# Kernel optimization log

Hardware: AMD Instinct MI355X
Metric: run time of the kernel (lower is better)

Reference implementation:

```python
import jax, jax.numpy as jnp
from jax import lax
import numpy as np

B = 4096          # batch
EMBED = 32        # embed_dim
HEADS = 2
MEM_SIZE = 4096
MEM_DIM = 256
TOPK = 10
LN_EPS = 1e-5


def setup_inputs() -> dict:
    key = jax.random.key(0)
    ks = jax.random.split(key, 32)
    rn = lambda i, shape, s=0.05: (jax.random.normal(ks[i], shape) * s).astype(jnp.float32)
    return {
        'x': jax.random.normal(ks[0], (B, 1, 28, 28), dtype=jnp.float32),
        'patch_w': rn(1, (32, 1, 4, 4)), 'patch_b': rn(2, (32,)),
        'blk_ln1_g': jnp.ones((2, 32), jnp.float32), 'blk_ln1_b': jnp.zeros((2, 32), jnp.float32),
        'blk_inproj_w': rn(3, (2, 96, 32)), 'blk_inproj_b': rn(4, (2, 96)),
        'blk_outproj_w': rn(5, (2, 32, 32)), 'blk_outproj_b': rn(6, (2, 32)),
        'blk_ln2_g': jnp.ones((2, 32), jnp.float32), 'blk_ln2_b': jnp.zeros((2, 32), jnp.float32),
        'blk_ff1_w': rn(7, (2, 128, 32)), 'blk_ff1_b': rn(8, (2, 128)),
        'blk_ff2_w': rn(9, (2, 32, 128)), 'blk_ff2_b': rn(10, (2, 32)),
        'lat_w': rn(11, (256, 1568)), 'lat_b': rn(12, (256,)),
        'memory': jax.random.normal(ks[13], (MEM_SIZE, MEM_DIM), dtype=jnp.float32),
        'dec_w': rn(14, (3136, 256)), 'dec_b': rn(15, (3136,)),
        'upt1_w': rn(16, (64, 32, 4, 4)), 'upt1_b': rn(17, (32,)),
        'c1_w': rn(18, (32, 32, 3, 3)), 'c1_b': rn(19, (32,)),
        'upt2_w': rn(20, (32, 16, 4, 4)), 'upt2_b': rn(21, (16,)),
        'c2_w': rn(22, (8, 16, 3, 3)), 'c2_b': rn(23, (8,)),
        'c3_w': rn(24, (1, 8, 1, 1)), 'c3_b': rn(25, (1,)),
    }


def _ln(x, g, b):
    m = jnp.mean(x, -1, keepdims=True)
    v = jnp.mean((x - m) ** 2, -1, keepdims=True)
    return (x - m) / jnp.sqrt(v + LN_EPS) * g + b


def _conv2d(x, w, b, stride=1, pad=0):
    out = lax.conv_general_dilated(x, w, (stride, stride), ((pad, pad), (pad, pad)),
                                   dimension_numbers=('NCHW', 'OIHW', 'NCHW'))
    return out + b[None, :, None, None]


def _conv_transpose2d(x, w, b, stride, pad):
    # w in torch layout [in, out, kh, kw]; equivalent fractionally-strided conv
    w_f = jnp.flip(w, (2, 3)).transpose(1, 0, 2, 3)  # OIHW
    k = w.shape[2]
    p = k - 1 - pad
    out = lax.conv_general_dilated(x, w_f, (1, 1), ((p, p), (p, p)),
                                   lhs_dilation=(stride, stride),
                                   dimension_numbers=('NCHW', 'OIHW', 'NCHW'))
    return out + b[None, :, None, None]


def _mha(x, wi, bi, wo, bo):
    Bn, S, D = x.shape
    Dh = D // HEADS
    qkv = x @ wi.T + bi                                  # [B,S,3D]
    q, k, v = jnp.split(qkv, 3, axis=-1)
    sp = lambda t: t.reshape(Bn, S, HEADS, Dh).transpose(0, 2, 1, 3)
    q, k, v = sp(q), sp(k), sp(v)
    scores = jnp.einsum('bhqd,bhkd->bhqk', q, k) / jnp.sqrt(jnp.asarray(Dh, x.dtype))
    att = jax.nn.softmax(scores, axis=-1)
    o = jnp.einsum('bhqk,bhkd->bhqd', att, v).transpose(0, 2, 1, 3).reshape(Bn, S, D)
    return o @ wo.T + bo


def _memory_read(latent, memory):
    # cosine-sim topk softmax-weighted gather (F.normalize eps=1e-12)
    mn = memory / jnp.clip(jnp.linalg.norm(memory, axis=1, keepdims=True), 1e-12)
    xn = latent / jnp.clip(jnp.linalg.norm(latent, axis=1, keepdims=True), 1e-12)
    sim = xn @ mn.T                                       # [B, MEM_SIZE]
    topk_sim, topk_idx = lax.top_k(sim, TOPK)
    w = jax.nn.softmax(topk_sim, axis=1)                  # [B, TOPK]
    sel = memory[topk_idx]                                # [B, TOPK, MEM_DIM]
    return jnp.einsum('bk,bkd->bd', w, sel)


def _forward(x, patch_w, patch_b, blk_ln1_g, blk_ln1_b, blk_inproj_w, blk_inproj_b,
             blk_outproj_w, blk_outproj_b, blk_ln2_g, blk_ln2_b, blk_ff1_w, blk_ff1_b,
             blk_ff2_w, blk_ff2_b, lat_w, lat_b, memory, dec_w, dec_b,
             upt1_w, upt1_b, c1_w, c1_b, upt2_w, upt2_b, c2_w, c2_b, c3_w, c3_b):
    Bn = x.shape[0]
    h = _conv2d(x, patch_w, patch_b, stride=4)            # [B,32,7,7]
    t = h.reshape(Bn, EMBED, 49).transpose(0, 2, 1)       # [B,49,32]
    for i in range(2):                                    # two SwinBlocks
        t = t + _mha(_ln(t, blk_ln1_g[i], blk_ln1_b[i]),
                     blk_inproj_w[i], blk_inproj_b[i], blk_outproj_w[i], blk_outproj_b[i])
        f = _ln(t, blk_ln2_g[i], blk_ln2_b[i])
        f = jax.nn.gelu(f @ blk_ff1_w[i].T + blk_ff1_b[i], approximate=False)
        t = t + (f @ blk_ff2_w[i].T + blk_ff2_b[i])
    latent = t.reshape(Bn, -1) @ lat_w.T + lat_b          # [B,256]
    mem_latent = _memory_read(latent, memory)             # [B,256]
    d = (mem_latent @ dec_w.T + dec_b).reshape(Bn, 64, 7, 7)  # dropout=eval identity
    d = jax.nn.relu(_conv_transpose2d(d, upt1_w, upt1_b, 2, 1))   # [B,32,14,14]
    d = jax.nn.relu(_conv2d(d, c1_w, c1_b, 1, 1))
    d = jax.nn.relu(_conv_transpose2d(d, upt2_w, upt2_b, 2, 1))   # [B,16,28,28]
    d = jax.nn.relu(_conv2d(d, c2_w, c2_b, 1, 1))                 # [B,8,28,28]
    return _conv2d(d, c3_w, c3_b, 1, 0)                           # [B,1,28,28]


def reference(x, patch_w, patch_b, blk_ln1_g, blk_ln1_b, blk_inproj_w, blk_inproj_b,
              blk_outproj_w, blk_outproj_b, blk_ln2_g, blk_ln2_b, blk_ff1_w, blk_ff1_b,
              blk_ff2_w, blk_ff2_b, lat_w, lat_b, memory, dec_w, dec_b,
              upt1_w, upt1_b, c1_w, c1_b, upt2_w, upt2_b, c2_w, c2_b, c3_w, c3_b):
    return _forward(x, patch_w, patch_b, blk_ln1_g, blk_ln1_b, blk_inproj_w, blk_inproj_b,
                    blk_outproj_w, blk_outproj_b, blk_ln2_g, blk_ln2_b, blk_ff1_w, blk_ff1_b,
                    blk_ff2_w, blk_ff2_b, lat_w, lat_b, memory, dec_w, dec_b,
                    upt1_w, upt1_b, c1_w, c1_b, upt2_w, upt2_b, c2_w, c2_b, c3_w, c3_b)
```

## Files before the change

### kernel.cpp

```cpp
#include <hip/hip_runtime.h>
#include <math.h>

#define B_TOT 4096
#define CHUNK 4096

typedef _Float16 half_t;
typedef _Float16 h2 __attribute__((ext_vector_type(2)));
typedef _Float16 h8v __attribute__((ext_vector_type(8)));
typedef float f4v __attribute__((ext_vector_type(4)));
typedef float f2v __attribute__((ext_vector_type(2)));

#if __has_builtin(__builtin_amdgcn_fdot2)
#define FDOT2(a, b, c) __builtin_amdgcn_fdot2((a), (b), (c), false)
#else
#define FDOT2(a, b, c) fmaf((float)(a)[1], (float)(b)[1], fmaf((float)(a)[0], (float)(b)[0], (c)))
#endif

#define KSTR 36
#define VSTR 34
#define KBYTES (49 * 72)
#define WAVE_LDS (49 * 72 + 49 * 136)
#define WI_OFF  (4 * WAVE_LDS)
#define BLOCK_LDS (WI_OFF + 12288)

__global__ __launch_bounds__(256) void k_tokens(
    const float* __restrict__ x, const float* __restrict__ pw, const float* __restrict__ pb,
    const float* __restrict__ ln1g, const float* __restrict__ ln1b,
    const float* __restrict__ wi, const float* __restrict__ bi,
    const float* __restrict__ wo, const float* __restrict__ bo,
    const float* __restrict__ ln2g, const float* __restrict__ ln2b,
    const float* __restrict__ w1, const float* __restrict__ fb1,
    const float* __restrict__ w2t, const float* __restrict__ fb2,
    float* __restrict__ tokens)
{
    __shared__ __align__(16) unsigned char Lraw[BLOCK_LDS];
    const int tid = threadIdx.x;
    const int wv = tid >> 6, lane = tid & 63;
    const int b = blockIdx.x * 4 + wv;
    half_t* Kb = (half_t*)(Lraw + wv * WAVE_LDS);
    float*  Vb = (float*)(Lraw + wv * WAVE_LDS + KBYTES);
    const float* wiL = (const float*)(Lraw + WI_OFF);
    float* Lf = (float*)Lraw;
    const bool is_tok = lane < 49;
    const int s = is_tok ? lane : 48;
    const int py = s / 7, px = s % 7;

    {
        const float4* srcw = (const float4*)(wi);
        float4* dstw = (float4*)(Lraw + WI_OFF);
        for (int e = tid; e < 768; e += 256) dstw[e] = srcw[e];
    }

    f2v xv2[8];
    const float* xb = x + (size_t)b * 784 + py * 112 + px * 4;
    #pragma unroll
    for (int r = 0; r < 4; ++r) {
        float4 vq = *(const float4*)(xb + r * 28);
        f2v lo; lo[0] = vq.x; lo[1] = vq.y;
        f2v hi; hi[0] = vq.z; hi[1] = vq.w;
        xv2[2 * r] = lo; xv2[2 * r + 1] = hi;
    }
    f2v t2[16];
    #pragma unroll
    for (int c = 0; c < 32; ++c) {
        const float* wr = pw + c * 16;
        f2v a2 = (f2v){0.f, 0.f};
        #pragma unroll
        for (int c2 = 0; c2 < 4; ++c2) {
            float4 wq = *(const float4*)&wr[4 * c2];
            f2v w0; w0[0] = wq.x; w0[1] = wq.y;
            f2v w1v; w1v[0] = wq.z; w1v[1] = wq.w;
            a2 += xv2[2 * c2] * w0;
            a2 += xv2[2 * c2 + 1] * w1v;
        }
        t2[c >> 1][c & 1] = pb[c] + a2[0] + a2[1];
    }

    for (int blk = 0; blk < 2; ++blk) {
        const float* bib = bi + blk * 96;

        f2v mu2 = (f2v){0.f, 0.f};
        #pragma unroll
        for (int i = 0; i < 16; ++i) mu2 += t2[i];
        float mu = (mu2[0] + mu2[1]) * 0.03125f;
        f2v mub; mub[0] = mu; mub[1] = mu;
        f2v var2 = (f2v){0.f, 0.f};
        #pragma unroll
        for (int i = 0; i < 16; ++i) { f2v d = t2[i] - mub; var2 += d * d; }
        float rstd = rsqrtf((var2[0] + var2[1]) * 0.03125f + 1e-5f);
        f2v rstd2; rstd2[0] = rstd; rstd2[1] = rstd;
        f2v xn2[16];
        {
            const f2v* g2 = (const f2v*)(ln1g + blk * 32);
            const f2v* bl2 = (const f2v*)(ln1b + blk * 32);
            #pragma unroll
            for (int i = 0; i < 16; ++i)
                xn2[i] = (t2[i] - mub) * rstd2 * g2[i] + bl2[i];
        }

        __syncthreads();

        #pragma unroll 4
        for (int d = 0; d < 32; ++d) {
            const float* wr = wiL + (32 + d) * 32;
            f2v a2 = (f2v){0.f, 0.f};
            #pragma unroll
            for (int c2 = 0; c2 < 8; ++c2) {
                float4 wq = *(const float4*)&wr[4 * c2];
                f2v w0; w0[0] = wq.x; w0[1] = wq.y;
                f2v w1v; w1v[0] = wq.z; w1v[1] = wq.w;
                a2 += xn2[2 * c2] * w0;
                a2 += xn2[2 * c2 + 1] * w1v;
            }
            if (is_tok) Kb[s * KSTR + d] = (half_t)(bib[32 + d] + a2[0] + a2[1]);
        }
        #pragma unroll 4
        for (int d = 0; d < 32; ++d) {
            const float* wr = wiL + (64 + d) * 32;
            f2v a2 = (f2v){0.f, 0.f};
            #pragma unroll
            for (int c2 = 0; c2 < 8; ++c2) {
                float4 wq = *(const float4*)&wr[4 * c2];
                f2v w0; w0[0] = wq.x; w0[1] = wq.y;
                f2v w1v; w1v[0] = wq.z; w1v[1] = wq.w;
                a2 += xn2[2 * c2] * w0;
                a2 += xn2[2 * c2 + 1] * w1v;
            }
            if (is_tok) Vb[s * VSTR + d] = bib[64 + d] + a2[0] + a2[1];
        }
        float q0[32];
        #pragma unroll 4
        for (int d = 0; d < 32; ++d) {
            const float* wr = wiL + d * 32;
            f2v a2 = (f2v){0.f, 0.f};
            #pragma unroll
            for (int c2 = 0; c2 < 8; ++c2) {
                float4 wq = *(const float4*)&wr[4 * c2];
                f2v w0; w0[0] = wq.x; w0[1] = wq.y;
                f2v w1v; w1v[0] = wq.z; w1v[1] = wq.w;
                a2 += xn2[2 * c2] * w0;
                a2 += xn2[2 * c2 + 1] * w1v;
            }
            q0[d] = (bib[d] + a2[0] + a2[1]) * 0.25f;
        }
        h2 qh[16];
        #pragma unroll
        for (int i = 0; i < 16; ++i) {
            h2 hh; hh[0] = (half_t)q0[2 * i]; hh[1] = (half_t)q0[2 * i + 1];
            qh[i] = hh;
        }

        __asm__ volatile("s_waitcnt lgkmcnt(0)" ::: "memory");

        f2v o2[16];
        #pragma unroll
        for (int i = 0; i < 16; ++i) o2[i] = (f2v){0.f, 0.f};
        float l0 = 0.f, l1 = 0.f;
        union H4 { double qd; h2 p[2]; };
        for (int j = 0; j < 49; ++j) {
            const double* kr = (const double*)(Kb + j * KSTR);
            const float* vr = Vb + j * VSTR;
            H4 u0, u1, u2, u3, w0, w1h, w2h, w3;
            u0.qd = kr[0]; u1.qd = kr[1]; u2.qd = kr[2]; u3.qd = kr[3];
            w0.qd = kr[4]; w1h.qd = kr[5]; w2h.qd = kr[6]; w3.qd = kr[7];
            float s0a = 0.f, s0b = 0.f, s1a = 0.f, s1b = 0.f;
            s0a = FDOT2(u0.p[0], qh[0], s0a); s0a = FDOT2(u0.p[1], qh[1], s0a);
            s0b = FDOT2(u1.p[0], qh[2], s0b); s0b = FDOT2(u1.p[1], qh[3], s0b);
            s0a = FDOT2(u2.p[0], qh[4], s0a); s0a = FDOT2(u2.p[1], qh[5], s0a);
            s0b = FDOT2(u3.p[0], qh[6], s0b); s0b = FDOT2(u3.p[1], qh[7], s0b);
            s1a = FDOT2(w0.p[0], qh[8], s1a); s1a = FDOT2(w0.p[1], qh[9], s1a);
            s1b = FDOT2(w1h.p[0], qh[10], s1b); s1b = FDOT2(w1h.p[1], qh[11], s1b);
            s1a = FDOT2(w2h.p[0], qh[12], s1a); s1a = FDOT2(w2h.p[1], qh[13], s1a);
            s1b = FDOT2(w3.p[0], qh[14], s1b); s1b = FDOT2(w3.p[1], qh[15], s1b);
            float p0 = __expf(s0a + s0b), p1 = __expf(s1a + s1b);
            l0 += p0; l1 += p1;
            f2v p02; p02[0] = p0; p02[1] = p0;
            f2v p12; p12[0] = p1; p12[1] = p1;
            #pragma unroll
            for (int i = 0; i < 8; ++i) {
                f2v va = *(const f2v*)&vr[2 * i];
                o2[i] += p02 * va;
                f2v vc = *(const f2v*)&vr[16 + 2 * i];
                o2[8 + i] += p12 * vc;
            }
        }
        {
            float il0 = 1.f / l0, il1 = 1.f / l1;
            f2v il02; il02[0] = il0; il02[1] = il0;
            f2v il12; il12[0] = il1; il12[1] = il1;
            #pragma unroll
            for (int i = 0; i < 8; ++i) { o2[i] *= il02; o2[8 + i] *= il12; }
        }

        #pragma unroll
        for (int c = 0; c < 32; ++c) {
            const float* wr = wo + blk * 1024 + c * 32;
            f2v a2 = (f2v){0.f, 0.f};
            #pragma unroll
            for (int c2 = 0; c2 < 8; ++c2) {
                float4 wq = *(const float4*)&wr[4 * c2];
                f2v w0; w0[0] = wq.x; w0[1] = wq.y;
                f2v w1v; w1v[0] = wq.z; w1v[1] = wq.w;
                a2 += o2[2 * c2] * w0;
                a2 += o2[2 * c2 + 1] * w1v;
            }
            t2[c >> 1][c & 1] += bo[blk * 32 + c] + a2[0] + a2[1];
        }

        mu2 = (f2v){0.f, 0.f};
        #pragma unroll
        for (int i = 0; i < 16; ++i) mu2 += t2[i];
        mu = (mu2[0] + mu2[1]) * 0.03125f;
        mub[0] = mu; mub[1] = mu;
        var2 = (f2v){0.f, 0.f};
        #pragma unroll
        for (int i = 0; i < 16; ++i) { f2v d = t2[i] - mub; var2 += d * d; }
        rstd = rsqrtf((var2[0] + var2[1]) * 0.03125f + 1e-5f);
        rstd2[0] = rstd; rstd2[1] = rstd;
        {
            const f2v* g2 = (const f2v*)(ln2g + blk * 32);
            const f2v* bl2 = (const f2v*)(ln2b + blk * 32);
            #pragma unroll
            for (int i = 0; i < 16; ++i)
                xn2[i] = (t2[i] - mub) * rstd2 * g2[i] + bl2[i];
        }

        __syncthreads();

        {
            const float4* src1 = (const float4*)(w1 + blk * 4096);
            const float4* src2 = (const float4*)(w2t + blk * 4096);
            float4* dst = (float4*)Lraw;
            for (int e = tid; e < 1024; e += 256) dst[e] = src1[e];
            for (int e = tid; e < 1024; e += 256) dst[1024 + e] = src2[e];
            if (blk == 0) {
                const float4* srcw = (const float4*)(wi + 3072);
                float4* dstw = (float4*)(Lraw + WI_OFF);
                for (int e = tid; e < 768; e += 256) dstw[e] = srcw[e];
            }
        }
        __syncthreads();

        const float* w2L = Lf + 4096;
        #pragma unroll 2
        for (int j = 0; j < 128; ++j) {
            const float* wr = Lf + j * 32;
            f2v h2a = (f2v){0.f, 0.f};
            #pragma unroll
            for (int c2 = 0; c2 < 8; ++c2) {
                float4 wq = *(const float4*)&wr[4 * c2];
                f2v w0; w0[0] = wq.x; w0[1] = wq.y;
                f2v w1v; w1v[0] = wq.z; w1v[1] = wq.w;
                h2a += xn2[2 * c2] * w0;
                h2a += xn2[2 * c2 + 1] * w1v;
            }
            float h = fb1[blk * 128 + j] + h2a[0] + h2a[1];
            h = 0.5f * h * (1.f + erff(h * 0.7071067811865476f));
            f2v hh; hh[0] = h; hh[1] = h;
            const float* w2r = w2L + j * 32;
            #pragma unroll
            for (int c2 = 0; c2 < 8; ++c2) {
                float4 wq = *(const float4*)&w2r[4 * c2];
                f2v w0; w0[0] = wq.x; w0[1] = wq.y;
                f2v w1v; w1v[0] = wq.z; w1v[1] = wq.w;
                t2[2 * c2]     += hh * w0;
                t2[2 * c2 + 1] += hh * w1v;
            }
        }
        {
            const f2v* fb22 = (const f2v*)(fb2 + blk * 32);
            #pragma unroll
            for (int i = 0; i < 16; ++i) t2[i] += fb22[i];
        }
    }

    if (is_tok) {
        float* op = tokens + (size_t)b * 1568 + s * 32;
        #pragma unroll
        for (int i = 0; i < 8; ++i) {
            float4 vv = make_float4(t2[2 * i][0], t2[2 * i][1],
                                    t2[2 * i + 1][0], t2[2 * i + 1][1]);
            *(float4*)&op[4 * i] = vv;
        }
    }
}

__global__ __launch_bounds__(256) void k_split(
    const float* __restrict__ lat_w, const float* __restrict__ memory,
    half_t* __restrict__ lwh, half_t* __restrict__ lwl,
    half_t* __restrict__ memh, half_t* __restrict__ meml)
{
    size_t i = (size_t)blockIdx.x * 256 + threadIdx.x;
    if (i < 401408) {
        float v = lat_w[i];
        half_t h = (half_t)v;
        lwh[i] = h; lwl[i] = (half_t)((v - (float)h) * 2048.0f);
    }
    if (i < 1048576) {
        float v = memory[i];
        half_t h = (half_t)v;
        memh[i] = h; meml[i] = (half_t)((v - (float)h) * 2048.0f);
    }
}

__global__ __launch_bounds__(256) void k_sgemm(
    const float* __restrict__ A, const half_t* __restrict__ Bhg,
    const half_t* __restrict__ Blg, const float* __restrict__ bias,
    float* __restrict__ C, int M, int N, int K)
{
    __shared__ __align__(16) half_t Ah[64 * 40];
    __shared__ __align__(16) half_t Al[64 * 40];
    __shared__ __align__(16) half_t Bh[128 * 40];
    __shared__ __align__(16) half_t Bl[128 * 40];
    const int tid = threadIdx.x;
    const int n0 = blockIdx.x * 128, m0 = blockIdx.y * 64;
    const int w = tid >> 6, lane = tid & 63;
    const int wm = (w >> 1) * 32, wn = (w & 1) * 64;
    const int lr = lane & 15, lk = lane >> 4;

    const int ar = tid >> 2, aseg = (tid & 3) * 8;
    const int br = tid >> 1, bseg = (tid & 1) * 16;

    f4v acch[2][4], accm[2][4];
    #pragma unroll
    for (int i = 0; i < 2; ++i)
        #pragma unroll
        for (int j = 0; j < 4; ++j) {
            acch[i][j] = (f4v){0.f, 0.f, 0.f, 0.f};
            accm[i][j] = (f4v){0.f, 0.f, 0.f, 0.f};
        }

    for (int k0 = 0; k0 < K; k0 += 32) {
        {
            const float* ap = A + (size_t)(m0 + ar) * K + k0 + aseg;
            float4 a0 = *(const float4*)ap;
            float4 a1 = *(const float4*)(ap + 4);
            float av[8] = {a0.x, a0.y, a0.z, a0.w, a1.x, a1.y, a1.z, a1.w};
            h8v ah, al;
            #pragma unroll
            for (int i = 0; i < 8; ++i) {
                half_t h = (half_t)av[i];
                ah[i] = h;
                al[i] = (half_t)((av[i] - (float)h) * 2048.0f);
            }
            *(h8v*)&Ah[ar * 40 + aseg] = ah;
            *(h8v*)&Al[ar * 40 + aseg] = al;

            const half_t* bph = Bhg + (size_t)(n0 + br) * K + k0 + bseg;
            const half_t* bpl = Blg + (size_t)(n0 + br) * K + k0 + bseg;
            h8v bh0 = *(const h8v*)bph;
            h8v bh1 = *(const h8v*)(bph + 8);
            h8v bl0 = *(const h8v*)bpl;
            h8v bl1 = *(const h8v*)(bpl + 8);
            *(h8v*)&Bh[br * 40 + bseg]     = bh0;
            *(h8v*)&Bh[br * 40 + bseg + 8] = bh1;
            *(h8v*)&Bl[br * 40 + bseg]     = bl0;
            *(h8v*)&Bl[br * 40 + bseg + 8] = bl1;
        }
        __syncthreads();
        h8v afh[2], afl[2], bfh[4], bfl[4];
        #pragma unroll
        for (int i = 0; i < 2; ++i) {
            afh[i] = *(const h8v*)&Ah[(wm + i * 16 + lr) * 40 + lk * 8];
            afl[i] = *(const h8v*)&Al[(wm + i * 16 + lr) * 40 + lk * 8];
        }
        #pragma unroll
        for (int j = 0; j < 4; ++j) {
            bfh[j] = *(const h8v*)&Bh[(wn + j * 16 + lr) * 40 + lk * 8];
            bfl[j] = *(const h8v*)&Bl[(wn + j * 16 + lr) * 40 + lk * 8];
        }
        #pragma unroll
        for (int i = 0; i < 2; ++i)
            #pragma unroll
            for (int j = 0; j < 4; ++j) {
                acch[i][j] = __builtin_amdgcn_mfma_f32_16x16x32_f16(afh[i], bfh[j], acch[i][j], 0, 0, 0);
                accm[i][j] = __builtin_amdgcn_mfma_f32_16x16x32_f16(afh[i], bfl[j], accm[i][j], 0, 0, 0);
                accm[i][j] = __builtin_amdgcn_mfma_f32_16x16x32_f16(afl[i], bfh[j], accm[i][j], 0, 0, 0);
            }
        __syncthreads();
    }

    #pragma unroll
    for (int j = 0; j < 4; ++j) {
        int n = n0 + wn + j * 16 + lr;
        float bv = bias ? bias[n] : 0.f;
        #pragma unroll
        for (int i = 0; i < 2; ++i) {
            #pragma unroll
            for (int r = 0; r < 4; ++r) {
                int m = m0 + wm + i * 16 + lk * 4 + r;
                C[(size_t)m * N + n] = acch[i][j][r] + accm[i][j][r] * (1.0f / 2048.0f) + bv;
            }
        }
    }
}

__global__ __launch_bounds__(256) void k_dgemm(
    const float* __restrict__ A, const float* __restrict__ Bm,
    const float* __restrict__ bias, half_t* __restrict__ C,
    int M, int N, int K)
{
    __shared__ __align__(16) half_t As[64 * 40];
    __shared__ __align__(16) half_t Bs[128 * 40];
    const int tid = threadIdx.x;
    const int n0 = blockIdx.x * 128, m0 = blockIdx.y * 64;
    const int w = tid >> 6, lane = tid & 63;
    const int wm = (w >> 1) * 32, wn = (w & 1) * 64;
    const int lr = lane & 15, lk = lane >> 4;

    const int ar = tid >> 2, aseg = (tid & 3) * 8;
    const int br = tid >> 1, bseg = (tid & 1) * 16;

    f4v acc[2][4];
    #pragma unroll
    for (int i = 0; i < 2; ++i)
        #pragma unroll
        for (int j = 0; j < 4; ++j) acc[i][j] = (f4v){0.f, 0.f, 0.f, 0.f};

    for (int k0 = 0; k0 < K; k0 += 32) {
        {
            const float* ap = A + (size_t)(m0 + ar) * K + k0 + aseg;
            float4 a0 = *(const float4*)ap;
            float4 a1 = *(const float4*)(ap + 4);
            h8v ha;
            ha[0] = (half_t)a0.x; ha[1] = (half_t)a0.y;
            ha[2] = (half_t)a0.z; ha[3] = (half_t)a0.w;
            ha[4] = (half_t)a1.x; ha[5] = (half_t)a1.y;
            ha[6] = (half_t)a1.z; ha[7] = (half_t)a1.w;
            *(h8v*)&As[ar * 40 + aseg] = ha;

            const float* bp = Bm + (size_t)(n0 + br) * K + k0 + bseg;
            float4 b0 = *(const float4*)bp;
            float4 b1 = *(const float4*)(bp + 4);
            float4 b2 = *(const float4*)(bp + 8);
            float4 b3 = *(const float4*)(bp + 12);
            h8v hb0, hb1;
            hb0[0] = (half_t)b0.x; hb0[1] = (half_t)b0.y;
            hb0[2] = (half_t)b0.z; hb0[3] = (half_t)b0.w;
            hb0[4] = (half_t)b1.x; hb0[5] = (half_t)b1.y;
            hb0[6] = (half_t)b1.z; hb0[7] = (half_t)b1.w;
            hb1[0] = (half_t)b2.x; hb1[1] = (half_t)b2.y;
            hb1[2] = (half_t)b2.z; hb1[3] = (half_t)b2.w;
            hb1[4] = (half_t)b3.x; hb1[5] = (half_t)b3.y;
            hb1[6] = (half_t)b3.z; hb1[7] = (half_t)b3.w;
            *(h8v*)&Bs[br * 40 + bseg] = hb0;
            *(h8v*)&Bs[br * 40 + bseg + 8] = hb1;
        }
        __syncthreads();
        h8v af[2], bfr[4];
        #pragma unroll
        for (int i = 0; i < 2; ++i)
            af[i] = *(const h8v*)&As[(wm + i * 16 + lr) * 40 + lk * 8];
        #pragma unroll
        for (int j = 0; j < 4; ++j)
            bfr[j] = *(const h8v*)&Bs[(wn + j * 16 + lr) * 40 + lk * 8];
        #pragma unroll
        for (int i = 0; i < 2; ++i)
            #pragma unroll
            for (int j = 0; j < 4; ++j)
                acc[i][j] = __builtin_amdgcn_mfma_f32_16x16x32_f16(af[i], bfr[j], acc[i][j], 0, 0, 0);
        __syncthreads();
    }

    #pragma unroll
    for (int j = 0; j < 4; ++j) {
        int n = n0 + wn + j * 16 + lr;
        float bv = bias[n];
        #pragma unroll
        for (int i = 0; i < 2; ++i) {
            #pragma unroll
            for (int r = 0; r < 4; ++r) {
                int m = m0 + wm + i * 16 + lk * 4 + r;
                C[(size_t)m * N + n] = (half_t)fmaxf(acc[i][j][r] + bv, 0.f);
            }
        }
    }
}

__global__ __launch_bounds__(256) void k_fuse(
    const float* __restrict__ wt1, const float* __restrict__ upt1_b,
    const float* __restrict__ dec_w, const float* __restrict__ dec_b,
    float* __restrict__ Wf, float* __restrict__ bf)
{
    __shared__ float WL[4][64][32];
    const int p = blockIdx.x;
    const int k = threadIdx.x;
    const int y = p / 14, x = p % 14;

    int ky0 = 0, iy0 = 0, ky1 = 0, iy1 = 0, nky = 0;
    for (int ky = 0; ky < 4; ++ky) {
        int iyn = y + 1 - ky;
        if (iyn < 0 || (iyn & 1)) continue;
        int iy = iyn >> 1;
        if (iy > 6) continue;
        if (nky == 0) { ky0 = ky; iy0 = iy; } else { ky1 = ky; iy1 = iy; }
        ++nky;
    }
    int kx0 = 0, ix0 = 0, kx1 = 0, ix1 = 0, nkx = 0;
    for (int kx = 0; kx < 4; ++kx) {
        int ixn = x + 1 - kx;
        if (ixn < 0 || (ixn & 1)) continue;
        int ix = ixn >> 1;
        if (ix > 6) continue;
        if (nkx == 0) { kx0 = kx; ix0 = ix; } else { kx1 = kx; ix1 = ix; }
        ++nkx;
    }
    const int ntap = nky * nkx;

    for (int e = k; e < ntap * 2048; e += 256) {
        int t = e >> 11, c = (e >> 5) & 63, o = e & 31;
        int ti = (nkx == 2) ? (t >> 1) : t;
        int tj = (nkx == 2) ? (t & 1) : 0;
        int ky = ti ? ky1 : ky0;
        int kx = tj ? kx1 : kx0;
        WL[t][c][o] = wt1[((c * 32 + o) * 4 + ky) * 4 + kx];
    }
    __syncthreads();

    f2v acc2[16];
    #pragma unroll
    for (int o = 0; o < 16; ++o) acc2[o] = (f2v){0.f, 0.f};
    float bacc = 0.f;

    for (int t = 0; t < ntap; ++t) {
        int ti = (nkx == 2) ? (t >> 1) : t;
        int tj = (nkx == 2) ? (t & 1) : 0;
        int iy = ti ? iy1 : iy0;
        int ix = tj ? ix1 : ix0;
        int rbase = iy * 7 + ix;
        for (int c = 0; c < 64; ++c) {
            int row = c * 49 + rbase;
            float v = dec_w[(size_t)row * 256 + k];
            f2v vv; vv[0] = v; vv[1] = v;
            const f2v* w2p = (const f2v*)&WL[t][c][0];
            #pragma unroll
            for (int o2 = 0; o2 < 16; ++o2) acc2[o2] += vv * w2p[o2];
            if (k < 32) bacc = fmaf(WL[t][c][k], dec_b[row], bacc);
        }
    }

    #pragma unroll 4
    for (int o = 0; o < 32; ++o)
        Wf[((size_t)(p * 32 + o)) * 256 + k] = acc2[o >> 1][o & 1];
    if (k < 32) bf[p * 32 + k] = bacc + upt1_b[k];
}

__global__ __launch_bounds__(256) void k_mnorm(const float* __restrict__ mem, float* __restrict__ inv_norm)
{
    __shared__ float red[256];
    const int row = blockIdx.x, tid = threadIdx.x;
    float v = mem[(size_t)row * 256 + tid];
    red[tid] = v * v;
    __syncthreads();
    for (int s = 128; s > 0; s >>= 1) {
        if (tid < s) red[tid] += red[tid + s];
        __syncthreads();
    }
    if (tid == 0) inv_norm[row] = 1.f / fmaxf(sqrtf(red[0]), 1e-12f);
}

__global__ __launch_bounds__(256) void k_memread(
    const float* __restrict__ latent, const float* __restrict__ dots,
    const float* __restrict__ inv_mn, const float* __restrict__ mem,
    float* __restrict__ out)
{
    __shared__ float red[256];
    __shared__ int   redi[4];
    __shared__ float inv_x_s;
    const int b = blockIdx.x, tid = threadIdx.x;
    const int w = tid >> 6, lane = tid & 63;
    float lx = latent[(size_t)b * 256 + tid];
    red[tid] = lx * lx;
    __syncthreads();
    for (int s = 128; s > 0; s >>= 1) {
        if (tid < s) red[tid] += red[tid + s];
        __syncthreads();
    }
    if (tid == 0) inv_x_s = 1.f / fmaxf(sqrtf(red[0]), 1e-12f);
    __syncthreads();
    const float inv_x = inv_x_s;

    float vals[16];
    for (int j = 0; j < 16; ++j) {
        int m = tid + j * 256;
        vals[j] = dots[(size_t)b * 4096 + m] * inv_mn[m] * inv_x;
    }
    float tv[10]; int ti[10];
    for (int t = 0; t < 10; ++t) {
        float bv = -1e30f; int bidx = 0x7fffffff;
        #pragma unroll
        for (int j = 0; j < 16; ++j) {
            int m = tid + j * 256;
            float v = vals[j];
            if (v > bv || (v == bv && m < bidx)) { bv = v; bidx = m; }
        }
        #pragma unroll
        for (int off = 32; off > 0; off >>= 1) {
            float ov = __shfl_xor(bv, off);
            int   oi = __shfl_xor(bidx, off);
            if (ov > bv || (ov == bv && oi < bidx)) { bv = ov; bidx = oi; }
        }
        if (lane == 0) { red[w] = bv; redi[w] = bidx; }
        __syncthreads();
        float fv = red[0]; int fi = redi[0];
        #pragma unroll
        for (int q = 1; q < 4; ++q) {
            float v2 = red[q]; int i2 = redi[q];
            if (v2 > fv || (v2 == fv && i2 < fi)) { fv = v2; fi = i2; }
        }
        tv[t] = fv; ti[t] = fi;
        if ((fi & 255) == tid) vals[fi >> 8] = -1e30f;
        __syncthreads();
    }
    float wgt[10], wsum = 0.f;
    for (int t = 0; t < 10; ++t) { wgt[t] = expf(tv[t] - tv[0]); wsum += wgt[t]; }
    float inv_ws = 1.f / wsum;
    float acc = 0.f;
    for (int t = 0; t < 10; ++t) acc += (wgt[t] * inv_ws) * mem[(size_t)ti[t] * 256 + tid];
    out[(size_t)b * 256 + tid] = acc;
}

__global__ __launch_bounds__(256) void k_pack(
    const float* __restrict__ wc1, const float* __restrict__ wt2,
    const float* __restrict__ wc2, const float* __restrict__ w2src,
    half_t* __restrict__ pk2h, half_t* __restrict__ pk3h,
    float* __restrict__ pk4, float* __restrict__ pk5)
{
    int i = blockIdx.x * 256 + threadIdx.x;
    if (i < 9216) {
        int ic = i & 31, oc = (i >> 5) & 15, nt = (i >> 9) & 1, t = i >> 10;
        pk2h[i] = (half_t)wc1[((nt * 16 + oc) * 32 + ic) * 9 + t];
    }
    if (i < 8192) {
        int ic = i & 31, oc = (i >> 5) & 15, t = (i >> 9) & 3, q = i >> 11;
        int wy = t >> 1, wx = t & 1, py = q >> 1, px = q & 1;
        int ky = 3 - py - 2 * wy, kx = 3 - px - 2 * wx;
        pk3h[i] = (half_t)wt2[((ic * 16 + oc) * 4 + ky) * 4 + kx];
    }
    if (i < 1152) {
        int o = i & 7, tap = (i >> 3) % 9, c = i / 72;
        pk4[i] = wc2[(o * 16 + c) * 9 + tap];
    }
    if (i < 8192) {
        int c = i & 31, j = (i >> 5) & 127, bq = i >> 12;
        pk5[i] = w2src[bq * 4096 + c * 128 + j];
    }
}

__global__ __launch_bounds__(256) void k_conv1(
    const half_t* __restrict__ in, const half_t* __restrict__ wh,
    const float* __restrict__ bias, half_t* __restrict__ out)
{
    __shared__ __align__(16) half_t P[2 * 16 * 16 * 40];
    const int tid = threadIdx.x;
    const int w = tid >> 6, lane = tid & 63;
    const size_t b0 = (size_t)blockIdx.x * 2;

    for (int e = tid; e < 10240; e += 256) ((unsigned int*)P)[e] = 0u;
    __syncthreads();
    {
        const unsigned int* src = (const unsigned int*)in;
        for (int e = tid; e < 6272; e += 256) {
            int si = e / 3136;
            int rem = e - si * 3136;
            int p = rem >> 4, c2 = rem & 15;
            int y = p / 14, x = p % 14;
            ((unsigned int*)P)[si * 5120 + ((y + 1) * 16 + (x + 1)) * 20 + c2] =
                src[(b0 + si) * 3136 + rem];
        }
    }

    h8v bfr[9][2];
    #pragma unroll
    for (int t = 0; t < 9; ++t)
        #pragma unroll
        for (int nt = 0; nt < 2; ++nt)
            bfr[t][nt] = *(const h8v*)&wh[((size_t)((t * 2 + nt) * 16 + (lane & 15))) * 32 + (lane >> 4) * 8];

    __syncthreads();

    const int kseg = (lane >> 4) * 8;
    const int oc = lane & 15;
    const float bv0 = bias[oc], bv1 = bias[16 + oc];

    for (int job = w; job < 26; job += 4) {
        const int si = job >= 13 ? 1 : 0;
        const int tile = job - si * 13;
        int p = tile * 16 + (lane & 15);
        if (p > 195) p = 195;
        const int y = p / 14, x = p % 14;
        const half_t* Pb = P + si * 10240;

        f4v acc0 = (f4v){0.f, 0.f, 0.f, 0.f};
        f4v acc1 = (f4v){0.f, 0.f, 0.f, 0.f};
        #pragma unroll
        for (int ky = 0; ky < 3; ++ky) {
            #pragma unroll
            for (int kx = 0; kx < 3; ++kx) {
                h8v af = *(const h8v*)&Pb[((y + ky) * 16 + (x + kx)) * 40 + kseg];
                acc0 = __builtin_amdgcn_mfma_f32_16x16x32_f16(af, bfr[ky * 3 + kx][0], acc0, 0, 0, 0);
                acc1 = __builtin_amdgcn_mfma_f32_16x16x32_f16(af, bfr[ky * 3 + kx][1], acc1, 0, 0, 0);
            }
        }

        const int pr0 = tile * 16 + (lane >> 4) * 4;
        half_t* ob = out + (b0 + si) * 6272;
        #pragma unroll
        for (int r = 0; r < 4; ++r) {
            int pp = pr0 + r;
            if (pp < 196) {
                ob[(size_t)pp * 32 + oc]      = (half_t)fmaxf(acc0[r] + bv0, 0.f);
                ob[(size_t)pp * 32 + 16 + oc] = (half_t)fmaxf(acc1[r] + bv1, 0.f);
            }
        }
    }
}

__global__ __launch_bounds__(256) void k_convt23(
    const half_t* __restrict__ in, const half_t* __restrict__ pk3h,
    const float* __restrict__ bt2, const float* __restrict__ pk4,
    const float* __restrict__ b2, const float* __restrict__ w3,
    const float* __restrict__ b3, float* __restrict__ out)
{
    __shared__ __align__(16) unsigned char Lraw[30720];
    half_t* Pin = (half_t*)Lraw;
    float*  P2  = (float*)Lraw;
    const int tid = threadIdx.x;
    const int w = tid >> 6, lane = tid & 63;
    const int b = blockIdx.x;

    for (int e = tid; e < 5120; e += 256) ((unsigned int*)Pin)[e] = 0u;
    __syncthreads();
    {
        const unsigned int* src = (const unsigned int*)in;
        for (int e = tid; e < 3136; e += 256) {
            int p = e >> 4, c2 = e & 15;
            int y = p / 14, x = p % 14;
            ((unsigned int*)Pin)[((y + 1) * 16 + (x + 1)) * 20 + c2] =
                src[(size_t)b * 3136 + e];
        }
    }
    __syncthreads();

    const int oc = lane & 15;
    const int kseg = (lane >> 4) * 8;

    f4v res[13];
    #pragma unroll
    for (int j = 0; j < 13; ++j) {
        const int job = w + 4 * j;
        const int q = job / 13, tile = job - q * 13;
        const int py = q >> 1, px = q & 1;
        int p = tile * 16 + (lane & 15);
        if (p > 195) p = 195;
        const int ty = p / 14, tx = p % 14;
        f4v a = (f4v){0.f, 0.f, 0.f, 0.f};
        #pragma unroll
        for (int t = 0; t < 4; ++t) {
            const int wy = t >> 1, wx = t & 1;
            h8v bf = *(const h8v*)&pk3h[((size_t)((q * 4 + t) * 16 + oc)) * 32 + kseg];
            h8v af = *(const h8v*)&Pin[((ty + py + wy) * 16 + (tx + px + wx)) * 40 + kseg];
            a = __builtin_amdgcn_mfma_f32_16x16x32_f16(af, bf, a, 0, 0, 0);
        }
        res[j] = a;
    }
    __syncthreads();

    const bool active2 = tid < 196;
    int row = active2 ? tid / 7 : 0;
    int tx0b = active2 ? (tid % 7) * 4 : 0;
    const float bco = bt2[oc];

    f2v acc2[4][4];
    #pragma unroll
    for (int i = 0; i < 4; ++i)
        #pragma unroll
        for (int o2 = 0; o2 < 4; ++o2) acc2[i][o2] = (f2v){0.f, 0.f};

    #pragma unroll
    for (int g = 0; g < 2; ++g) {
        for (int e = tid; e < 7680; e += 256) P2[e] = 0.f;
        __syncthreads();
        if ((oc >> 3) == g) {
            #pragma unroll
            for (int j = 0; j < 13; ++j) {
                const int job = w + 4 * j;
                const int q = job / 13, tile = job - q * 13;
                const int py = q >> 1, px = q & 1;
                const int pr0 = tile * 16 + (lane >> 4) * 4;
                #pragma unroll
                for (int r = 0; r < 4; ++r) {
                    int p = pr0 + r;
                    if (p < 196) {
                        int Y = 2 * (p / 14) + py, X = 2 * (p % 14) + px;
                        P2[((oc & 7) * 30 + Y + 1) * 32 + (X + 1)] = fmaxf(res[j][r] + bco, 0.f);
                    }
                }
            }
        }
        __syncthreads();
        for (int cl = 0; cl < 8; ++cl) {
            const float* Pb = &P2[(cl * 30 + row) * 32 + tx0b];
            const float* wb = pk4 + (size_t)(g * 8 + cl) * 72;
            #pragma unroll
            for (int ky = 0; ky < 3; ++ky) {
                float4 a = *(const float4*)&Pb[ky * 32];
                float4 bq = *(const float4*)&Pb[ky * 32 + 4];
                float rowb[8] = {a.x, a.y, a.z, a.w, bq.x, bq.y, bq.z, bq.w};
                #pragma unroll
                for (int kx = 0; kx < 3; ++kx) {
                    const f2v* wt2p = (const f2v*)(wb + (ky * 3 + kx) * 8);
                    #pragma unroll
                    for (int i = 0; i < 4; ++i) {
                        f2v rb; rb[0] = rowb[i + kx]; rb[1] = rowb[i + kx];
                        acc2[i][0] += rb * wt2p[0];
                        acc2[i][1] += rb * wt2p[1];
                        acc2[i][2] += rb * wt2p[2];
                        acc2[i][3] += rb * wt2p[3];
                    }
                }
            }
        }
        __syncthreads();
    }

    if (active2) {
        const float bias3 = b3[0];
        #pragma unroll
        for (int i = 0; i < 4; ++i) {
            float r = bias3;
            #pragma unroll
            for (int o = 0; o < 8; ++o)
                r += fmaxf(acc2[i][o >> 1][o & 1] + b2[o], 0.f) * w3[o];
            out[(size_t)b * 784 + row * 28 + tx0b + i] = r;
        }
    }
}

extern "C" void kernel_launch(void* const* d_in, const int* in_sizes, int n_in,
                              void* d_out, int out_size, void* d_ws, size_t ws_size,
                              hipStream_t stream)
{
    const float* x       = (const float*)d_in[0];
    const float* patch_w = (const float*)d_in[1];
    const float* patch_b = (const float*)d_in[2];
    const float* ln1g    = (const float*)d_in[3];
    const float* ln1b    = (const float*)d_in[4];
    const float* wi      = (const float*)d_in[5];
    const float* bi      = (const float*)d_in[6];
    const float* wo      = (const float*)d_in[7];
    const float* bo      = (const float*)d_in[8];
    const float* ln2g    = (const float*)d_in[9];
    const float* ln2b    = (const float*)d_in[10];
    const float* w1      = (const float*)d_in[11];
    const float* b1      = (const float*)d_in[12];
    const float* w2      = (const float*)d_in[13];
    const float* b2      = (const float*)d_in[14];
    const float* lat_w   = (const float*)d_in[15];
    const float* lat_b   = (const float*)d_in[16];
    const float* memory  = (const float*)d_in[17];
    const float* dec_w   = (const float*)d_in[18];
    const float* dec_b   = (const float*)d_in[19];
    const float* upt1_w  = (const float*)d_in[20];
    const float* upt1_b  = (const float*)d_in[21];
    const float* c1_w    = (const float*)d_in[22];
    const float* c1_b    = (const float*)d_in[23];
    const float* upt2_w  = (const float*)d_in[24];
    const float* upt2_b  = (const float*)d_in[25];
    const float* c2_w    = (const float*)d_in[26];
    const float* c2_b    = (const float*)d_in[27];
    const float* c3_w    = (const float*)d_in[28];
    const float* c3_b    = (const float*)d_in[29];
    float* outp = (float*)d_out;

    float* ws = (float*)d_ws;
    size_t off = 0;
    auto alloc = [&](size_t n) { float* p = ws + off; off += (n + 63) & ~(size_t)63; return p; };
    float* tokens     = alloc((size_t)B_TOT * 1568);
    float* latent     = alloc((size_t)B_TOT * 256);
    float* dots       = alloc((size_t)B_TOT * 4096);
    float* mem_latent = alloc((size_t)B_TOT * 256);
    float* inv_mn     = alloc(4096);
    half_t* pk2h      = (half_t*)alloc(4608);
    half_t* pk3h      = (half_t*)alloc(4096);
    float* pk4        = alloc(1152);
    float* pk5        = alloc(8192);
    float* Wf         = alloc((size_t)6272 * 256);
    float* bf         = alloc(6272);
    half_t* d1h       = (half_t*)alloc((size_t)CHUNK * 6272 / 2);
    half_t* d2h       = (half_t*)alloc((size_t)CHUNK * 6272 / 2);
    half_t* lwh       = (half_t*)alloc(200704);
    half_t* lwl       = (half_t*)alloc(200704);
    half_t* memh      = (half_t*)alloc(524288);
    half_t* meml      = (half_t*)alloc(524288);
    (void)in_sizes; (void)n_in; (void)out_size; (void)ws_size;

    k_pack<<<36, 256, 0, stream>>>(c1_w, upt2_w, c2_w, w2, pk2h, pk3h, pk4, pk5);
    k_split<<<4096, 256, 0, stream>>>(lat_w, memory, lwh, lwl, memh, meml);
    k_fuse<<<196, 256, 0, stream>>>(upt1_w, upt1_b, dec_w, dec_b, Wf, bf);

    k_tokens<<<B_TOT / 4, 256, 0, stream>>>(x, patch_w, patch_b, ln1g, ln1b, wi, bi,
                                            wo, bo, ln2g, ln2b, w1, b1, pk5, b2, tokens);
    k_sgemm<<<dim3(256 / 128, B_TOT / 64), 256, 0, stream>>>(tokens, lwh, lwl, lat_b,
                                                             latent, B_TOT, 256, 1568);
    k_mnorm<<<4096, 256, 0, stream>>>(memory, inv_mn);
    k_sgemm<<<dim3(4096 / 128, B_TOT / 64), 256, 0, stream>>>(latent, memh, meml, nullptr,
                                                              dots, B_TOT, 4096, 256);
    k_memread<<<B_TOT, 256, 0, stream>>>(latent, dots, inv_mn, memory, mem_latent);

    for (int c = 0; c < B_TOT / CHUNK; ++c) {
        const float* ml = mem_latent + (size_t)c * CHUNK * 256;
        k_dgemm<<<dim3(6272 / 128, CHUNK / 64), 256, 0, stream>>>(ml, Wf, bf, d1h,
                                                                  CHUNK, 6272, 256);
        k_conv1  <<<CHUNK / 2, 256, 0, stream>>>(d1h, pk2h, c1_b, d2h);
        k_convt23<<<CHUNK, 256, 0, stream>>>(d2h, pk3h, upt2_b, pk4, c2_b, c3_w, c3_b,
                                             outp + (size_t)c * CHUNK * 784);
    }
}
```

Before: 1.050 ms.

## Fuse memory row-norm into split kernel and read attention weights from global

The memory-row inverse-norm reduction is folded into k_split, which already loads each memory element, so the separate k_mnorm launch and its second read of memory are dropped. Separately, k_tokens stops staging the in-projection weights in LDS and reads them directly from global (cached) memory. This shrinks per-block LDS, which may allow more blocks per CU. The cost is that the weight loads are now served by the caches instead of LDS.

New measurement: 1.115 ms. +6.2%, slower.

```diff
diff --git a/kernel.cpp b/kernel.cpp
--- a/kernel.cpp
+++ b/kernel.cpp
@@ -20,8 +20,7 @@
 #define VSTR 34
 #define KBYTES (49 * 72)
 #define WAVE_LDS (49 * 72 + 49 * 136)
-#define WI_OFF  (4 * WAVE_LDS)
-#define BLOCK_LDS (WI_OFF + 12288)
+#define BLOCK_LDS (4 * WAVE_LDS)
 
 __global__ __launch_bounds__(256) void k_tokens(
     const float* __restrict__ x, const float* __restrict__ pw, const float* __restrict__ pb,
@@ -39,17 +38,10 @@
     const int b = blockIdx.x * 4 + wv;
     half_t* Kb = (half_t*)(Lraw + wv * WAVE_LDS);
     float*  Vb = (float*)(Lraw + wv * WAVE_LDS + KBYTES);
-    const float* wiL = (const float*)(Lraw + WI_OFF);
     float* Lf = (float*)Lraw;
     const bool is_tok = lane < 49;
     const int s = is_tok ? lane : 48;
     const int py = s / 7, px = s % 7;
-
-    {
-        const float4* srcw = (const float4*)(wi);
-        float4* dstw = (float4*)(Lraw + WI_OFF);
-        for (int e = tid; e < 768; e += 256) dstw[e] = srcw[e];
-    }
 
     f2v xv2[8];
     const float* xb = x + (size_t)b * 784 + py * 112 + px * 4;
@@ -78,6 +70,7 @@
 
     for (int blk = 0; blk < 2; ++blk) {
         const float* bib = bi + blk * 96;
+        const float* wib = wi + blk * 3072;
 
         f2v mu2 = (f2v){0.f, 0.f};
         #pragma unroll
@@ -102,7 +95,7 @@
 
         #pragma unroll 4
         for (int d = 0; d < 32; ++d) {
-            const float* wr = wiL + (32 + d) * 32;
+            const float* wr = wib + (32 + d) * 32;
             f2v a2 = (f2v){0.f, 0.f};
             #pragma unroll
             for (int c2 = 0; c2 < 8; ++c2) {
@@ -116,7 +109,7 @@
         }
         #pragma unroll 4
         for (int d = 0; d < 32; ++d) {
-            const float* wr = wiL + (64 + d) * 32;
+            const float* wr = wib + (64 + d) * 32;
             f2v a2 = (f2v){0.f, 0.f};
             #pragma unroll
             for (int c2 = 0; c2 < 8; ++c2) {
@@ -131,7 +124,7 @@
         float q0[32];
         #pragma unroll 4
         for (int d = 0; d < 32; ++d) {
-            const float* wr = wiL + d * 32;
+            const float* wr = wib + d * 32;
             f2v a2 = (f2v){0.f, 0.f};
             #pragma unroll
             for (int c2 = 0; c2 < 8; ++c2) {
@@ -233,11 +226,6 @@
             float4* dst = (float4*)Lraw;
             for (int e = tid; e < 1024; e += 256) dst[e] = src1[e];
             for (int e = tid; e < 1024; e += 256) dst[1024 + e] = src2[e];
-            if (blk == 0) {
-                const float4* srcw = (const float4*)(wi + 3072);
-                float4* dstw = (float4*)(Lraw + WI_OFF);
-                for (int e = tid; e < 768; e += 256) dstw[e] = srcw[e];
-            }
         }
         __syncthreads();
 
@@ -288,18 +276,31 @@
 __global__ __launch_bounds__(256) void k_split(
     const float* __restrict__ lat_w, const float* __restrict__ memory,
     half_t* __restrict__ lwh, half_t* __restrict__ lwl,
-    half_t* __restrict__ memh, half_t* __restrict__ meml)
+    half_t* __restrict__ memh, half_t* __restrict__ meml,
+    float* __restrict__ inv_norm)
 {
-    size_t i = (size_t)blockIdx.x * 256 + threadIdx.x;
+    __shared__ float red[256];
+    const int tid = threadIdx.x;
+    size_t i = (size_t)blockIdx.x * 256 + tid;
     if (i < 401408) {
         float v = lat_w[i];
         half_t h = (half_t)v;
         lwh[i] = h; lwl[i] = (half_t)((v - (float)h) * 2048.0f);
     }
+    float v = 0.f;
     if (i < 1048576) {
-        float v = memory[i];
+        v = memory[i];
         half_t h = (half_t)v;
         memh[i] = h; meml[i] = (half_t)((v - (float)h) * 2048.0f);
+    }
+    if (blockIdx.x < 4096) {
+        red[tid] = v * v;
+        __syncthreads();
+        for (int s = 128; s > 0; s >>= 1) {
+            if (tid < s) red[tid] += red[tid + s];
+            __syncthreads();
+        }
+        if (tid == 0) inv_norm[blockIdx.x] = 1.f / fmaxf(sqrtf(red[0]), 1e-12f);
     }
 }
 
@@ -543,20 +544,6 @@
     for (int o = 0; o < 32; ++o)
         Wf[((size_t)(p * 32 + o)) * 256 + k] = acc2[o >> 1][o & 1];
     if (k < 32) bf[p * 32 + k] = bacc + upt1_b[k];
-}
-
-__global__ __launch_bounds__(256) void k_mnorm(const float* __restrict__ mem, float* __restrict__ inv_norm)
-{
-    __shared__ float red[256];
-    const int row = blockIdx.x, tid = threadIdx.x;
-    float v = mem[(size_t)row * 256 + tid];
-    red[tid] = v * v;
-    __syncthreads();
-    for (int s = 128; s > 0; s >>= 1) {
-        if (tid < s) red[tid] += red[tid + s];
-        __syncthreads();
-    }
-    if (tid == 0) inv_norm[row] = 1.f / fmaxf(sqrtf(red[0]), 1e-12f);
 }
 
 __global__ __launch_bounds__(256) void k_memread(
@@ -896,14 +883,13 @@
     (void)in_sizes; (void)n_in; (void)out_size; (void)ws_size;
 
     k_pack<<<36, 256, 0, stream>>>(c1_w, upt2_w, c2_w, w2, pk2h, pk3h, pk4, pk5);
-    k_split<<<4096, 256, 0, stream>>>(lat_w, memory, lwh, lwl, memh, meml);
+    k_split<<<4096, 256, 0, stream>>>(lat_w, memory, lwh, lwl, memh, meml, inv_mn);
     k_fuse<<<196, 256, 0, stream>>>(upt1_w, upt1_b, dec_w, dec_b, Wf, bf);
 
     k_tokens<<<B_TOT / 4, 256, 0, stream>>>(x, patch_w, patch_b, ln1g, ln1b, wi, bi,
                                             wo, bo, ln2g, ln2b, w1, b1, pk5, b2, tokens);
     k_sgemm<<<dim3(256 / 128, B_TOT / 64), 256, 0, stream>>>(tokens, lwh, lwl, lat_b,
                                                              latent, B_TOT, 256, 1568);
-    k_mnorm<<<4096, 256, 0, stream>>>(memory, inv_mn);
     k_sgemm<<<dim3(4096 / 128, B_TOT / 64), 256, 0, stream>>>(latent, memh, meml, nullptr,
                                                               dots, B_TOT, 4096, 256);
     k_memread<<<B_TOT, 256, 0, stream>>>(latent, dots, inv_mn, memory, mem_latent);
```
